# Optimization experiments

Measured on AMD Instinct MI355X. Metric: run time of the kernel, lower is better.

## Reference

```python
import jax, jax.numpy as jnp
import numpy as np

NEG_SLOPE = 0.2

def gat_layer(x, src, dst, W, b, a_src, a_dst, heads, out_dim, concat):
    N = x.shape[0]
    h = (x @ W).reshape(N, heads, out_dim)            # [N,H,D]
    s_src = jnp.sum(h * a_src, axis=-1)               # [N,H]
    s_dst = jnp.sum(h * a_dst, axis=-1)               # [N,H]
    e = jax.nn.leaky_relu(s_src[src] + s_dst[dst], NEG_SLOPE)  # [E,H]
    # segment softmax over destination nodes (self-loops guarantee nonempty segments)
    m = jax.ops.segment_max(e, dst, num_segments=N)
    e = jnp.exp(e - m[dst])
    denom = jax.ops.segment_sum(e, dst, num_segments=N)
    alpha = e / denom[dst]                            # [E,H]
    msg = h[src] * alpha[:, :, None]                  # [E,H,D]
    out = jax.ops.segment_sum(msg, dst, num_segments=N)  # [N,H,D]
    if concat:
        out = out.reshape(N, heads * out_dim)
    else:
        out = out.mean(axis=1)
    return out + b

def setup_inputs() -> dict:
    key = jax.random.key(0)
    ks = jax.random.split(key, 16)
    N, E = 50000, 1600000
    IN, HID, OUT, H = 128, 256, 32, 4
    D = HID // H
    def glorot(k, shape):
        fan = shape[0] + shape[-1]
        return jax.random.uniform(k, shape, jnp.float32, -1.0, 1.0) * np.sqrt(6.0 / fan)
    x = jax.random.normal(ks[0], (N, IN), jnp.float32)
    edge_index = jax.random.randint(ks[1], (2, E), 0, N, jnp.int32)
    return {
        "x": x, "edge_index": edge_index,
        "W0": glorot(ks[2], (IN, H * D)), "b0": jnp.zeros((H * D,), jnp.float32),
        "asrc0": glorot(ks[3], (H, D)), "adst0": glorot(ks[4], (H, D)),
        "W1": glorot(ks[5], (HID, H * D)), "b1": jnp.zeros((H * D,), jnp.float32),
        "asrc1": glorot(ks[6], (H, D)), "adst1": glorot(ks[7], (H, D)),
        "W2": glorot(ks[8], (HID, 1 * OUT)), "b2": jnp.zeros((OUT,), jnp.float32),
        "asrc2": glorot(ks[9], (1, OUT)), "adst2": glorot(ks[10], (1, OUT)),
    }

def reference(x, edge_index, W0, b0, asrc0, adst0, W1, b1, asrc1, adst1, W2, b2, asrc2, adst2):
    N = x.shape[0]
    # add self-loops (PyG GATConv default)
    loop = jnp.arange(N, dtype=edge_index.dtype)
    src = jnp.concatenate([edge_index[0], loop])
    dst = jnp.concatenate([edge_index[1], loop])
    h = gat_layer(x, src, dst, W0, b0, asrc0, adst0, heads=4, out_dim=64, concat=True)
    h = jax.nn.elu(h)
    h = gat_layer(h, src, dst, W1, b1, asrc1, adst1, heads=4, out_dim=64, concat=True)
    h = jax.nn.elu(h)
    h = gat_layer(h, src, dst, W2, b2, asrc2, adst2, heads=1, out_dim=32, concat=False)
    return jax.nn.log_softmax(h, axis=1)
```

## Files before the change

### kernel.cpp

```cpp
#include <hip/hip_runtime.h>
#include <hip/hip_bf16.h>
#include <math.h>

#define IN_DIM 128
#define HID    256
#define OUTD   32
#define HEADS  4
#define NB_SH  7
#define BUCKET_CAP 6144
#define NCHUNK_BLKS 256

typedef __attribute__((ext_vector_type(8))) short s8v;
typedef __attribute__((ext_vector_type(4))) float f4v;

__device__ inline unsigned short f2bf(float f) {
    union { __hip_bfloat16 b; unsigned short u; } cv;
    cv.b = __float2bfloat16(f);
    return cv.u;
}


__global__ __launch_bounds__(256) void csr_hist(const int* __restrict__ ei,
                                                int* __restrict__ H,
                                                int E, int N, int NB, int per_blk) {
    __shared__ int hist[512];
    int t = threadIdx.x;
    for (int i = t; i < NB; i += 256) hist[i] = 0;
    __syncthreads();
    int lo = blockIdx.x * per_blk;
    int hi = min(lo + per_blk, E + N);
    for (int e = lo + t; e < hi; e += 256) {
        int dst = (e < E) ? ei[E + e] : (e - E);
        atomicAdd(&hist[dst >> NB_SH], 1);
    }
    __syncthreads();
    for (int i = t; i < NB; i += 256) H[blockIdx.x * NB + i] = hist[i];
}

__global__ __launch_bounds__(256) void csr_colscan(int* __restrict__ H,
                                                   int* __restrict__ total, int NB) {
    int b = blockIdx.x, t = threadIdx.x;
    int v = H[t * NB + b];
    __shared__ int s[256];
    s[t] = v;
    __syncthreads();
    for (int o = 1; o < 256; o <<= 1) {
        int x = (t >= o) ? s[t - o] : 0;
        __syncthreads();
        s[t] += x;
        __syncthreads();
    }
    H[t * NB + b] = s[t] - v;
    if (t == 255) total[b] = s[255];
}

__global__ void csr_basescan(const int* __restrict__ total, int* __restrict__ base, int NB) {
    __shared__ int s[512];
    int t = threadIdx.x;
    int v = (t < NB) ? total[t] : 0;
    s[t] = v;
    __syncthreads();
    for (int o = 1; o < 512; o <<= 1) {
        int x = (t >= o) ? s[t - o] : 0;
        __syncthreads();
        s[t] += x;
        __syncthreads();
    }
    if (t < NB) base[t] = s[t] - v;
    if (t == NB - 1) base[NB] = s[t];
}

__global__ __launch_bounds__(256) void csr_partition(const int* __restrict__ ei,
                                                     const int* __restrict__ H,
                                                     const int* __restrict__ base,
                                                     int* __restrict__ ebuf,
                                                     int E, int N, int per_blk, int NB) {
    __shared__ int cur[512];
    int t = threadIdx.x;
    for (int i = t; i < NB; i += 256) cur[i] = base[i] + H[blockIdx.x * NB + i];
    __syncthreads();
    int lo = blockIdx.x * per_blk;
    int hi = min(lo + per_blk, E + N);
    for (int e = lo + t; e < hi; e += 256) {
        int src = (e < E) ? ei[e] : (e - E);
        int dst = (e < E) ? ei[E + e] : (e - E);
        int pos = atomicAdd(&cur[dst >> NB_SH], 1);
        ebuf[pos] = src | ((dst & 127) << 16);
    }
}

__global__ __launch_bounds__(256) void csr_sort(const int* __restrict__ ebuf,
                                                const int* __restrict__ base,
                                                int* __restrict__ col,
                                                int* __restrict__ rp, int N, int NB) {
    int b = blockIdx.x, t = threadIdx.x;
    int lo = base[b], hi = base[b + 1];
    int nbase = b << NB_SH;
    __shared__ int c_[128], sc[128], cur[128];
    __shared__ int loc[BUCKET_CAP];
    if (t < 128) c_[t] = 0;
    __syncthreads();
    for (int k = lo + t; k < hi; k += 256) atomicAdd(&c_[(ebuf[k] >> 16) & 127], 1);
    __syncthreads();
    if (t < 128) sc[t] = c_[t];
    __syncthreads();
    for (int o = 1; o < 128; o <<= 1) {
        int x = 0;
        if (t < 128 && t >= o) x = sc[t - o];
        __syncthreads();
        if (t < 128) sc[t] += x;
        __syncthreads();
    }
    if (t < 128) {
        int excl = sc[t] - c_[t];
        cur[t] = excl;
        int node = nbase + t;
        if (node < N) rp[node] = lo + excl;
    }
    if (b == NB - 1 && t == 0) rp[N] = hi;
    __syncthreads();
    for (int k = lo + t; k < hi; k += 256) {
        int e = ebuf[k];
        int p = atomicAdd(&cur[(e >> 16) & 127], 1);
        if (p < BUCKET_CAP) loc[p] = e & 0xFFFF;
    }
    __syncthreads();
    int m = min(hi - lo, BUCKET_CAP);
    for (int k = t; k < m; k += 256) col[lo + k] = loc[k];
}


__global__ __launch_bounds__(256) void prep_w(const float* __restrict__ W,
                                              unsigned short* __restrict__ Wt_h,
                                              unsigned short* __restrict__ Wt_l,
                                              int K, int N) {
    int idx = blockIdx.x * 256 + threadIdx.x;
    if (idx >= K * N) return;
    int n = idx / K, k = idx % K;
    float x = W[(size_t)k * N + n];
    unsigned short h = f2bf(x);
    float hf = __uint_as_float((unsigned)h << 16);
    Wt_h[idx] = h;
    Wt_l[idx] = f2bf(x - hf);
}

__global__ __launch_bounds__(256) void prep_x(const float* __restrict__ X,
                                              unsigned short* __restrict__ Xh,
                                              unsigned short* __restrict__ Xl,
                                              int total8) {
    int idx = blockIdx.x * 256 + threadIdx.x;
    if (idx >= total8) return;
    size_t b = (size_t)idx * 8;
    float4 v0 = *(const float4*)(X + b);
    float4 v1 = *(const float4*)(X + b + 4);
    float x[8] = {v0.x, v0.y, v0.z, v0.w, v1.x, v1.y, v1.z, v1.w};
    union { unsigned short s[8]; uint4 q; } h, l;
#pragma unroll
    for (int j = 0; j < 8; j++) {
        h.s[j] = f2bf(x[j]);
        l.s[j] = f2bf(x[j] - __uint_as_float((unsigned)h.s[j] << 16));
    }
    *(uint4*)(Xh + b) = h.q;
    *(uint4*)(Xl + b) = l.q;
}


template <int BN>
__global__ __launch_bounds__(256, 2) void gemm_mfma(const unsigned short* __restrict__ Ah,
                                                    const unsigned short* __restrict__ Al,
                                                    const unsigned short* __restrict__ Wt_h,
                                                    const unsigned short* __restrict__ Wt_l,
                                                    unsigned short* __restrict__ Cb,
                                                    const float* __restrict__ asrc,
                                                    const float* __restrict__ adst,
                                                    float* __restrict__ ssrcO,
                                                    float* __restrict__ sdstO,
                                                    int M, int K, int Nst, int Hn) {
    constexpr int WROWS = (BN == 128) ? 64 : 32;
    constexpr int WCOLS = (BN == 128) ? 64 : 32;
    constexpr int MI = WROWS / 16, NJ = WCOLS / 16;
    __shared__ unsigned short As_h[128][64], As_l[128][64];
    __shared__ unsigned short Bs_h[BN][64], Bs_l[BN][64];
    int tid = threadIdx.x;
    int lane = tid & 63, w = tid >> 6;
    int wm, wn;
    if (BN == 128) { wm = w & 1; wn = w >> 1; } else { wm = w; wn = 0; }
    int row0 = blockIdx.x * 128, col0 = blockIdx.y * BN;

    f4v acc[MI][NJ];
#pragma unroll
    for (int i = 0; i < MI; i++)
#pragma unroll
        for (int j = 0; j < NJ; j++) acc[i][j] = (f4v)(0.f);

    for (int k0 = 0; k0 < K; k0 += 64) {
#pragma unroll
        for (int i = 0; i < 4; i++) {
            int cidx = tid + i * 256;
            int r = cidx >> 3, ch = cidx & 7;
            int grow = row0 + r;
            uint4 vh = make_uint4(0, 0, 0, 0), vl = make_uint4(0, 0, 0, 0);
            if (grow < M) {
                size_t g = (size_t)grow * K + k0 + ch * 8;
                vh = *(const uint4*)(Ah + g);
                vl = *(const uint4*)(Al + g);
            }
            int chs = ch ^ (r & 7);
            *(uint4*)&As_h[r][chs * 8] = vh;
            *(uint4*)&As_l[r][chs * 8] = vl;
        }
#pragma unroll
        for (int i = 0; i < BN * 8 / 256; i++) {
            int cidx = tid + i * 256;
            int n = cidx >> 3, ch = cidx & 7;
            int chs = ch ^ (n & 7);
            size_t g = (size_t)(col0 + n) * K + k0 + ch * 8;
            *(uint4*)&Bs_h[n][chs * 8] = *(const uint4*)(Wt_h + g);
            *(uint4*)&Bs_l[n][chs * 8] = *(const uint4*)(Wt_l + g);
        }
        __syncthreads();
#pragma unroll
        for (int ks = 0; ks < 2; ks++) {
            s8v ah[MI], al[MI], bh[NJ], bl[NJ];
            int kc = ks * 4 + (lane >> 4);
            int lr = lane & 15;
#pragma unroll
            for (int i = 0; i < MI; i++) {
                int r = wm * WROWS + i * 16 + lr;
                ah[i] = *(const s8v*)&As_h[r][(kc ^ (r & 7)) * 8];
                al[i] = *(const s8v*)&As_l[r][(kc ^ (r & 7)) * 8];
            }
#pragma unroll
            for (int j = 0; j < NJ; j++) {
                int n = wn * WCOLS + j * 16 + lr;
                bh[j] = *(const s8v*)&Bs_h[n][(kc ^ (n & 7)) * 8];
                bl[j] = *(const s8v*)&Bs_l[n][(kc ^ (n & 7)) * 8];
            }
#pragma unroll
            for (int i = 0; i < MI; i++)
#pragma unroll
                for (int j = 0; j < NJ; j++) {
                    acc[i][j] = __builtin_amdgcn_mfma_f32_16x16x32_bf16(ah[i], bh[j], acc[i][j], 0, 0, 0);
                    acc[i][j] = __builtin_amdgcn_mfma_f32_16x16x32_bf16(ah[i], bl[j], acc[i][j], 0, 0, 0);
                    acc[i][j] = __builtin_amdgcn_mfma_f32_16x16x32_bf16(al[i], bh[j], acc[i][j], 0, 0, 0);
                }
        }
        __syncthreads();
    }
    int lr = lane & 15, lg = lane >> 4;
#pragma unroll
    for (int i = 0; i < MI; i++)
#pragma unroll
        for (int j = 0; j < NJ; j++) {
            int gcol = col0 + wn * WCOLS + j * 16 + lr;
#pragma unroll
            for (int rr = 0; rr < 4; rr++) {
                int grow = row0 + wm * WROWS + i * 16 + lg * 4 + rr;
                if (grow < M) Cb[(size_t)grow * Nst + gcol] = f2bf(acc[i][j][rr]);
            }
        }
    int hd = (BN == 128) ? (blockIdx.y * 2 + wn) : 0;
    float as_[NJ], ad_[NJ];
#pragma unroll
    for (int j = 0; j < NJ; j++) {
        int gcol = col0 + wn * WCOLS + j * 16 + lr;
        as_[j] = asrc[gcol];
        ad_[j] = adst[gcol];
    }
#pragma unroll
    for (int i = 0; i < MI; i++)
#pragma unroll
        for (int rr = 0; rr < 4; rr++) {
            float ps = 0.f, pd = 0.f;
#pragma unroll
            for (int j = 0; j < NJ; j++) {
                ps += acc[i][j][rr] * as_[j];
                pd += acc[i][j][rr] * ad_[j];
            }
#pragma unroll
            for (int off = 1; off < 16; off <<= 1) {
                ps += __shfl_xor(ps, off);
                pd += __shfl_xor(pd, off);
            }
            int grow = row0 + wm * WROWS + i * 16 + lg * 4 + rr;
            if (lr == 0 && grow < M) {
                ssrcO[(size_t)grow * Hn + hd] = ps;
                sdstO[(size_t)grow * Hn + hd] = pd;
            }
        }
}


template <int CH, int H, int MODE, int UNR>
__global__ __launch_bounds__(256) void gat_fused(const unsigned short* __restrict__ hb,
                                                 const float* __restrict__ ssrc,
                                                 const float* __restrict__ sdst,
                                                 const int* __restrict__ rp,
                                                 const int* __restrict__ col,
                                                 const float* __restrict__ bias,
                                                 float* __restrict__ outF,
                                                 unsigned short* __restrict__ outH,
                                                 unsigned short* __restrict__ outL, int N) {
    const int TPE = CH / 8;
    const int EPW = 64 / TPE;
    const int D = CH / H;
    constexpr int SHCH = (CH == 256) ? 9 : 6;
    constexpr int SHS = (H == 4) ? 4 : 2;
    int wv = threadIdx.x >> 6, lane = threadIdx.x & 63;
    int n = blockIdx.x * 4 + wv;
    if (n >= N) return;
    int k0 = __builtin_amdgcn_readfirstlane(rp[n]);
    int k1 = __builtin_amdgcn_readfirstlane(rp[n + 1]);

    int h1 = lane % H;
    int slot = lane / H;
    const int SL = 64 / H;
    float sd1 = sdst[(size_t)n * H + h1];
    float m = -1e30f, l = 0.f;
    for (int k = k0 + slot; k < k1; k += SL) {
        int s = col[k];
        float e = ssrc[(size_t)s * H + h1] + sd1;
        e = (e > 0.f) ? e : 0.2f * e;
        float mn = fmaxf(m, e);
        l = l * __expf(m - mn) + __expf(e - mn);
        m = mn;
    }
#pragma unroll
    for (int off = H; off < 64; off <<= 1) {
        float m2 = __shfl_xor(m, off);
        float l2 = __shfl_xor(l, off);
        float mn = fmaxf(m, m2);
        l = l * __expf(m - mn) + l2 * __expf(m2 - mn);
        m = mn;
    }

    int eo = lane / TPE;
    int c = (lane % TPE) * 8;
    int head = c / D;
    float mh = __shfl(m, head);
    float invl = 1.f / __shfl(l, head);
    float sdh = __shfl(sd1, head);

    const char* hbc = (const char*)hb;
    const char* ssc = (const char*)ssrc;
    unsigned cb = (unsigned)(c << 1);
    unsigned hb4 = (unsigned)(head << 2);

    float acc[8];
#pragma unroll
    for (int j = 0; j < 8; j++) acc[j] = 0.f;

    for (int k = k0; k < k1; k += UNR * EPW) {
        int ss[UNR];
        float aa[UNR];
#pragma unroll
        for (int u = 0; u < UNR; u++) {
            int ku = k + u * EPW + eo;
            bool v = ku < k1;
            ss[u] = col[v ? ku : k0];
            aa[u] = v ? invl : 0.f;
        }
        uint4 hv[UNR];
#pragma unroll
        for (int u = 0; u < UNR; u++)
            hv[u] = *(const uint4*)(hbc + (((unsigned)ss[u] << SHCH) + cb));
#pragma unroll
        for (int u = 0; u < UNR; u++) {
            float e = *(const float*)(ssc + (((unsigned)ss[u] << SHS) + hb4)) + sdh;
            e = (e > 0.f) ? e : 0.2f * e;
            aa[u] *= __expf(e - mh);
        }
#pragma unroll
        for (int u = 0; u < UNR; u++) {
            const unsigned* p = (const unsigned*)&hv[u];
#pragma unroll
            for (int q = 0; q < 4; q++) {
                acc[2 * q]     += aa[u] * __uint_as_float(p[q] << 16);
                acc[2 * q + 1] += aa[u] * __uint_as_float(p[q] & 0xffff0000u);
            }
        }
    }
#pragma unroll
    for (int off = TPE; off < 64; off <<= 1)
#pragma unroll
        for (int j = 0; j < 8; j++) acc[j] += __shfl_xor(acc[j], off);

    float o[8];
#pragma unroll
    for (int j = 0; j < 8; j++) o[j] = acc[j] + bias[c + j];
    if (MODE == 1) {
        float mx = o[0];
#pragma unroll
        for (int j = 1; j < 8; j++) mx = fmaxf(mx, o[j]);
#pragma unroll
        for (int off = 1; off < TPE; off <<= 1) mx = fmaxf(mx, __shfl_xor(mx, off));
        float sm = 0.f;
#pragma unroll
        for (int j = 0; j < 8; j++) sm += __expf(o[j] - mx);
#pragma unroll
        for (int off = 1; off < TPE; off <<= 1) sm += __shfl_xor(sm, off);
        float lg = logf(sm) + mx;
        if (eo != 0) return;
        float4* op = (float4*)(outF + (size_t)n * CH + c);
        op[0] = make_float4(o[0] - lg, o[1] - lg, o[2] - lg, o[3] - lg);
        op[1] = make_float4(o[4] - lg, o[5] - lg, o[6] - lg, o[7] - lg);
    } else {
        if (eo != 0) return;
        union { unsigned short s[8]; uint4 q; } ph, pl;
#pragma unroll
        for (int j = 0; j < 8; j++) {
            float v = (o[j] > 0.f) ? o[j] : expm1f(o[j]);
            ph.s[j] = f2bf(v);
            pl.s[j] = f2bf(v - __uint_as_float((unsigned)ph.s[j] << 16));
        }
        *(uint4*)(outH + (size_t)n * CH + c) = ph.q;
        *(uint4*)(outL + (size_t)n * CH + c) = pl.q;
    }
}


extern "C" void kernel_launch(void* const* d_in, const int* in_sizes, int n_in,
                              void* d_out, int out_size, void* d_ws, size_t ws_size,
                              hipStream_t stream) {
    const float* x   = (const float*)d_in[0];
    const int*   ei  = (const int*)d_in[1];
    const float* W0  = (const float*)d_in[2];
    const float* b0  = (const float*)d_in[3];
    const float* as0 = (const float*)d_in[4];
    const float* ad0 = (const float*)d_in[5];
    const float* W1  = (const float*)d_in[6];
    const float* b1  = (const float*)d_in[7];
    const float* as1 = (const float*)d_in[8];
    const float* ad1 = (const float*)d_in[9];
    const float* W2  = (const float*)d_in[10];
    const float* b2  = (const float*)d_in[11];
    const float* as2 = (const float*)d_in[12];
    const float* ad2 = (const float*)d_in[13];

    int N = in_sizes[0] / IN_DIM;
    int E = in_sizes[1] / 2;
    int Et = E + N;
    int NB = (N + 127) >> NB_SH;

    char* w = (char*)d_ws;
    size_t off = 0;
    auto alloc = [&](size_t bytes) -> void* {
        void* p = w + off;
        off = (off + bytes + 255) & ~(size_t)255;
        return p;
    };
    unsigned short* Qh    = (unsigned short*)alloc((size_t)N * HID * 2);
    unsigned short* Ql    = (unsigned short*)alloc((size_t)N * HID * 2);
    unsigned short* Ab    = (unsigned short*)alloc((size_t)N * HID * 2);
    unsigned short* xh    = (unsigned short*)alloc((size_t)N * IN_DIM * 2);
    unsigned short* xl    = (unsigned short*)alloc((size_t)N * IN_DIM * 2);
    float*          ssrc  = (float*)alloc((size_t)N * HEADS * 4);
    float*          sdst  = (float*)alloc((size_t)N * HEADS * 4);
    int*            rp    = (int*)alloc((size_t)(N + 1) * 4);
    int*            col   = (int*)alloc((size_t)Et * 4);
    int*            H     = (int*)alloc((size_t)NCHUNK_BLKS * NB * 4);
    int*            total = (int*)alloc((size_t)(NB + 1) * 4);
    int*            base  = (int*)alloc((size_t)(NB + 1) * 4);
    int*            ebuf  = (int*)alloc((size_t)Et * 4);
    unsigned short* Wt0h  = (unsigned short*)alloc((size_t)IN_DIM * HID * 2);
    unsigned short* Wt0l  = (unsigned short*)alloc((size_t)IN_DIM * HID * 2);
    unsigned short* Wt1h  = (unsigned short*)alloc((size_t)HID * HID * 2);
    unsigned short* Wt1l  = (unsigned short*)alloc((size_t)HID * HID * 2);
    unsigned short* Wt2h  = (unsigned short*)alloc((size_t)HID * OUTD * 2);
    unsigned short* Wt2l  = (unsigned short*)alloc((size_t)HID * OUTD * 2);

    prep_w<<<(IN_DIM * HID + 255) / 256, 256, 0, stream>>>(W0, Wt0h, Wt0l, IN_DIM, HID);
    prep_w<<<(HID * HID + 255) / 256, 256, 0, stream>>>(W1, Wt1h, Wt1l, HID, HID);
    prep_w<<<(HID * OUTD + 255) / 256, 256, 0, stream>>>(W2, Wt2h, Wt2l, HID, OUTD);
    int t8 = N * IN_DIM / 8;
    prep_x<<<(t8 + 255) / 256, 256, 0, stream>>>(x, xh, xl, t8);

    int per_blk = (Et + NCHUNK_BLKS - 1) / NCHUNK_BLKS;
    csr_hist<<<NCHUNK_BLKS, 256, 0, stream>>>(ei, H, E, N, NB, per_blk);
    csr_colscan<<<NB, 256, 0, stream>>>(H, total, NB);
    csr_basescan<<<1, 512, 0, stream>>>(total, base, NB);
    csr_partition<<<NCHUNK_BLKS, 256, 0, stream>>>(ei, H, base, ebuf, E, N, per_blk, NB);
    csr_sort<<<NB, 256, 0, stream>>>(ebuf, base, col, rp, N, NB);

    dim3 gm((N + 127) / 128, 2);
    dim3 gm2((N + 127) / 128, 1);
    int gg = (N + 3) / 4;

    gemm_mfma<128><<<gm, 256, 0, stream>>>(xh, xl, Wt0h, Wt0l, Ab, as0, ad0, ssrc, sdst,
                                           N, IN_DIM, HID, HEADS);
    gat_fused<HID, HEADS, 0, 6><<<gg, 256, 0, stream>>>(Ab, ssrc, sdst, rp, col, b0,
                                                        nullptr, Qh, Ql, N);

    gemm_mfma<128><<<gm, 256, 0, stream>>>(Qh, Ql, Wt1h, Wt1l, Ab, as1, ad1, ssrc, sdst,
                                           N, HID, HID, HEADS);
    gat_fused<HID, HEADS, 0, 6><<<gg, 256, 0, stream>>>(Ab, ssrc, sdst, rp, col, b1,
                                                        nullptr, Qh, Ql, N);

    gemm_mfma<32><<<gm2, 256, 0, stream>>>(Qh, Ql, Wt2h, Wt2l, Ab, as2, ad2, ssrc, sdst,
                                           N, HID, OUTD, 1);
    gat_fused<OUTD, 1, 1, 2><<<gg, 256, 0, stream>>>(Ab, ssrc, sdst, rp, col, b2,
                                                     (float*)d_out, nullptr, nullptr, N);
}
```

Baseline: 430.3 us.

## Process attention heads sequentially per wave in fused GAT aggregation

The aggregation kernel now loops over heads, and within each head the wave's lanes cover only that head's D features, so more edges are processed per pass (TPE = D/8 instead of CH/8). Each lane loads one head's score per edge rather than mixing heads across lanes, and the unroll factor for the hidden layers drops from 6 to 2. The edge list and column indices are now re-read once per head, adding more load instructions and more loop overhead. In exchange, each pass covers more edges in parallel, and smaller rows may improve locality per head.

```diff
diff --git a/kernel.cpp b/kernel.cpp
--- a/kernel.cpp
+++ b/kernel.cpp
@@ -301,11 +301,9 @@
                                                  float* __restrict__ outF,
                                                  unsigned short* __restrict__ outH,
                                                  unsigned short* __restrict__ outL, int N) {
-    const int TPE = CH / 8;
+    const int D = CH / H;
+    const int TPE = D / 8;
     const int EPW = 64 / TPE;
-    const int D = CH / H;
-    constexpr int SHCH = (CH == 256) ? 9 : 6;
-    constexpr int SHS = (H == 4) ? 4 : 2;
     int wv = threadIdx.x >> 6, lane = threadIdx.x & 63;
     int n = blockIdx.x * 4 + wv;
     if (n >= N) return;
@@ -335,86 +333,87 @@
     }
 
     int eo = lane / TPE;
-    int c = (lane % TPE) * 8;
-    int head = c / D;
-    float mh = __shfl(m, head);
-    float invl = 1.f / __shfl(l, head);
-    float sdh = __shfl(sd1, head);
-
-    const char* hbc = (const char*)hb;
-    const char* ssc = (const char*)ssrc;
-    unsigned cb = (unsigned)(c << 1);
-    unsigned hb4 = (unsigned)(head << 2);
-
-    float acc[8];
-#pragma unroll
-    for (int j = 0; j < 8; j++) acc[j] = 0.f;
-
-    for (int k = k0; k < k1; k += UNR * EPW) {
-        int ss[UNR];
-        float aa[UNR];
-#pragma unroll
-        for (int u = 0; u < UNR; u++) {
-            int ku = k + u * EPW + eo;
-            bool v = ku < k1;
-            ss[u] = col[v ? ku : k0];
-            aa[u] = v ? invl : 0.f;
-        }
-        uint4 hv[UNR];
-#pragma unroll
-        for (int u = 0; u < UNR; u++)
-            hv[u] = *(const uint4*)(hbc + (((unsigned)ss[u] << SHCH) + cb));
-#pragma unroll
-        for (int u = 0; u < UNR; u++) {
-            float e = *(const float*)(ssc + (((unsigned)ss[u] << SHS) + hb4)) + sdh;
-            e = (e > 0.f) ? e : 0.2f * e;
-            aa[u] *= __expf(e - mh);
-        }
-#pragma unroll
-        for (int u = 0; u < UNR; u++) {
-            const unsigned* p = (const unsigned*)&hv[u];
-#pragma unroll
-            for (int q = 0; q < 4; q++) {
-                acc[2 * q]     += aa[u] * __uint_as_float(p[q] << 16);
-                acc[2 * q + 1] += aa[u] * __uint_as_float(p[q] & 0xffff0000u);
-            }
-        }
-    }
-#pragma unroll
-    for (int off = TPE; off < 64; off <<= 1)
-#pragma unroll
-        for (int j = 0; j < 8; j++) acc[j] += __shfl_xor(acc[j], off);
-
-    float o[8];
-#pragma unroll
-    for (int j = 0; j < 8; j++) o[j] = acc[j] + bias[c + j];
-    if (MODE == 1) {
-        float mx = o[0];
-#pragma unroll
-        for (int j = 1; j < 8; j++) mx = fmaxf(mx, o[j]);
-#pragma unroll
-        for (int off = 1; off < TPE; off <<= 1) mx = fmaxf(mx, __shfl_xor(mx, off));
-        float sm = 0.f;
-#pragma unroll
-        for (int j = 0; j < 8; j++) sm += __expf(o[j] - mx);
-#pragma unroll
-        for (int off = 1; off < TPE; off <<= 1) sm += __shfl_xor(sm, off);
-        float lg = logf(sm) + mx;
-        if (eo != 0) return;
-        float4* op = (float4*)(outF + (size_t)n * CH + c);
-        op[0] = make_float4(o[0] - lg, o[1] - lg, o[2] - lg, o[3] - lg);
-        op[1] = make_float4(o[4] - lg, o[5] - lg, o[6] - lg, o[7] - lg);
-    } else {
-        if (eo != 0) return;
-        union { unsigned short s[8]; uint4 q; } ph, pl;
-#pragma unroll
-        for (int j = 0; j < 8; j++) {
-            float v = (o[j] > 0.f) ? o[j] : expm1f(o[j]);
-            ph.s[j] = f2bf(v);
-            pl.s[j] = f2bf(v - __uint_as_float((unsigned)ph.s[j] << 16));
-        }
-        *(uint4*)(outH + (size_t)n * CH + c) = ph.q;
-        *(uint4*)(outL + (size_t)n * CH + c) = pl.q;
+    int cl = (lane % TPE) * 8;
+
+    for (int hd = 0; hd < H; hd++) {
+        float mh = __shfl(m, hd);
+        float invl = 1.f / __shfl(l, hd);
+        float sdh = __shfl(sd1, hd);
+        int c = hd * D + cl;
+
+        float acc[8];
+#pragma unroll
+        for (int j = 0; j < 8; j++) acc[j] = 0.f;
+
+        for (int k = k0; k < k1; k += UNR * EPW) {
+            int ss[UNR];
+            float aa[UNR];
+#pragma unroll
+            for (int u = 0; u < UNR; u++) {
+                int ku = k + u * EPW + eo;
+                bool v = ku < k1;
+                ss[u] = col[v ? ku : k0];
+                aa[u] = v ? invl : 0.f;
+            }
+            uint4 hv[UNR];
+#pragma unroll
+            for (int u = 0; u < UNR; u++)
+                hv[u] = *(const uint4*)(hb + (size_t)ss[u] * CH + c);
+#pragma unroll
+            for (int u = 0; u < UNR; u++) {
+                float e = ssrc[(size_t)ss[u] * H + hd] + sdh;
+                e = (e > 0.f) ? e : 0.2f * e;
+                aa[u] *= __expf(e - mh);
+            }
+#pragma unroll
+            for (int u = 0; u < UNR; u++) {
+                const unsigned* p = (const unsigned*)&hv[u];
+#pragma unroll
+                for (int q = 0; q < 4; q++) {
+                    acc[2 * q]     += aa[u] * __uint_as_float(p[q] << 16);
+                    acc[2 * q + 1] += aa[u] * __uint_as_float(p[q] & 0xffff0000u);
+                }
+            }
+        }
+#pragma unroll
+        for (int off = TPE; off < 64; off <<= 1)
+#pragma unroll
+            for (int j = 0; j < 8; j++) acc[j] += __shfl_xor(acc[j], off);
+
+        if (MODE == 1) {
+            float o[8];
+#pragma unroll
+            for (int j = 0; j < 8; j++) o[j] = acc[j] + bias[c + j];
+            float mx = o[0];
+#pragma unroll
+            for (int j = 1; j < 8; j++) mx = fmaxf(mx, o[j]);
+#pragma unroll
+            for (int off = 1; off < TPE; off <<= 1) mx = fmaxf(mx, __shfl_xor(mx, off));
+            float sm = 0.f;
+#pragma unroll
+            for (int j = 0; j < 8; j++) sm += __expf(o[j] - mx);
+#pragma unroll
+            for (int off = 1; off < TPE; off <<= 1) sm += __shfl_xor(sm, off);
+            float lg = logf(sm) + mx;
+            if (eo == 0) {
+                float4* op = (float4*)(outF + (size_t)n * CH + c);
+                op[0] = make_float4(o[0] - lg, o[1] - lg, o[2] - lg, o[3] - lg);
+                op[1] = make_float4(o[4] - lg, o[5] - lg, o[6] - lg, o[7] - lg);
+            }
+        } else {
+            if (eo == 0) {
+                union { unsigned short s[8]; uint4 q; } ph, pl;
+#pragma unroll
+                for (int j = 0; j < 8; j++) {
+                    float v = acc[j] + bias[c + j];
+                    v = (v > 0.f) ? v : expm1f(v);
+                    ph.s[j] = f2bf(v);
+                    pl.s[j] = f2bf(v - __uint_as_float((unsigned)ph.s[j] << 16));
+                }
+                *(uint4*)(outH + (size_t)n * CH + c) = ph.q;
+                *(uint4*)(outL + (size_t)n * CH + c) = pl.q;
+            }
+        }
     }
 }
 
@@ -488,12 +487,12 @@
 
     gemm_mfma<128><<<gm, 256, 0, stream>>>(xh, xl, Wt0h, Wt0l, Ab, as0, ad0, ssrc, sdst,
                                            N, IN_DIM, HID, HEADS);
-    gat_fused<HID, HEADS, 0, 6><<<gg, 256, 0, stream>>>(Ab, ssrc, sdst, rp, col, b0,
+    gat_fused<HID, HEADS, 0, 2><<<gg, 256, 0, stream>>>(Ab, ssrc, sdst, rp, col, b0,
                                                         nullptr, Qh, Ql, N);
 
     gemm_mfma<128><<<gm, 256, 0, stream>>>(Qh, Ql, Wt1h, Wt1l, Ab, as1, ad1, ssrc, sdst,
                                            N, HID, HID, HEADS);
-    gat_fused<HID, HEADS, 0, 6><<<gg, 256, 0, stream>>>(Ab, ssrc, sdst, rp, col, b1,
+    gat_fused<HID, HEADS, 0, 2><<<gg, 256, 0, stream>>>(Ab, ssrc, sdst, rp, col, b1,
                                                         nullptr, Qh, Ql, N);
 
     gemm_mfma<32><<<gm2, 256, 0, stream>>>(Qh, Ql, Wt2h, Wt2l, Ab, as2, ad2, ssrc, sdst,
```

After: 547.6 us. 27.3% more time.

## Sort CSR column indices by source range within each destination row

Applied to the files above, without the earlier changes.

The bucket sort in csr_sort now keys on (destination node, coarse source bin), so neighbor lists inside each row are grouped by source-index range. The aim is better cache locality for the gathers of source features in the aggregation kernels. The counting array grows to 128*64 shared ints, and the scan becomes a 256-thread block scan over 32-entry chunks, which adds some sort cost. The gat_fused template parameter for the two hidden layers also drops from 6 to 4.

```diff
diff --git a/kernel.cpp b/kernel.cpp
--- a/kernel.cpp
+++ b/kernel.cpp
@@ -9,6 +9,8 @@
 #define NB_SH  7
 #define BUCKET_CAP 6144
 #define NCHUNK_BLKS 256
+#define SRC_SH 10
+#define KSRC   64
 
 typedef __attribute__((ext_vector_type(8))) short s8v;
 typedef __attribute__((ext_vector_type(4))) float f4v;
@@ -96,32 +98,47 @@
     int b = blockIdx.x, t = threadIdx.x;
     int lo = base[b], hi = base[b + 1];
     int nbase = b << NB_SH;
-    __shared__ int c_[128], sc[128], cur[128];
+    __shared__ int cnt[128 * KSRC];
     __shared__ int loc[BUCKET_CAP];
-    if (t < 128) c_[t] = 0;
-    __syncthreads();
-    for (int k = lo + t; k < hi; k += 256) atomicAdd(&c_[(ebuf[k] >> 16) & 127], 1);
-    __syncthreads();
-    if (t < 128) sc[t] = c_[t];
-    __syncthreads();
-    for (int o = 1; o < 128; o <<= 1) {
-        int x = 0;
-        if (t < 128 && t >= o) x = sc[t - o];
-        __syncthreads();
-        if (t < 128) sc[t] += x;
-        __syncthreads();
-    }
-    if (t < 128) {
-        int excl = sc[t] - c_[t];
-        cur[t] = excl;
-        int node = nbase + t;
-        if (node < N) rp[node] = lo + excl;
-    }
-    if (b == NB - 1 && t == 0) rp[N] = hi;
+    __shared__ int ssum[256];
+    for (int i = t; i < 128 * KSRC; i += 256) cnt[i] = 0;
     __syncthreads();
     for (int k = lo + t; k < hi; k += 256) {
         int e = ebuf[k];
-        int p = atomicAdd(&cur[(e >> 16) & 127], 1);
+        int key = ((e >> 16) & 127) * KSRC + ((e & 0xFFFF) >> SRC_SH);
+        atomicAdd(&cnt[key], 1);
+    }
+    __syncthreads();
+    int base_i = t * 32;
+    int s = 0;
+#pragma unroll
+    for (int i = 0; i < 32; i++) s += cnt[base_i + i];
+    ssum[t] = s;
+    __syncthreads();
+    for (int o = 1; o < 256; o <<= 1) {
+        int x = (t >= o) ? ssum[t - o] : 0;
+        __syncthreads();
+        ssum[t] += x;
+        __syncthreads();
+    }
+    int run = (t == 0) ? 0 : ssum[t - 1];
+#pragma unroll
+    for (int i = 0; i < 32; i++) {
+        int c = cnt[base_i + i];
+        cnt[base_i + i] = run;
+        run += c;
+    }
+    __syncthreads();
+    if (t < 128) {
+        int node = nbase + t;
+        if (node < N) rp[node] = lo + cnt[t * KSRC];
+    }
+    if (b == NB - 1 && t == 0) rp[N] = hi;
+    __syncthreads();
+    for (int k = lo + t; k < hi; k += 256) {
+        int e = ebuf[k];
+        int key = ((e >> 16) & 127) * KSRC + ((e & 0xFFFF) >> SRC_SH);
+        int p = atomicAdd(&cnt[key], 1);
         if (p < BUCKET_CAP) loc[p] = e & 0xFFFF;
     }
     __syncthreads();
@@ -488,12 +505,12 @@
 
     gemm_mfma<128><<<gm, 256, 0, stream>>>(xh, xl, Wt0h, Wt0l, Ab, as0, ad0, ssrc, sdst,
                                            N, IN_DIM, HID, HEADS);
-    gat_fused<HID, HEADS, 0, 6><<<gg, 256, 0, stream>>>(Ab, ssrc, sdst, rp, col, b0,
+    gat_fused<HID, HEADS, 0, 4><<<gg, 256, 0, stream>>>(Ab, ssrc, sdst, rp, col, b0,
                                                         nullptr, Qh, Ql, N);
 
     gemm_mfma<128><<<gm, 256, 0, stream>>>(Qh, Ql, Wt1h, Wt1l, Ab, as1, ad1, ssrc, sdst,
                                            N, HID, HID, HEADS);
-    gat_fused<HID, HEADS, 0, 6><<<gg, 256, 0, stream>>>(Ab, ssrc, sdst, rp, col, b1,
+    gat_fused<HID, HEADS, 0, 4><<<gg, 256, 0, stream>>>(Ab, ssrc, sdst, rp, col, b1,
                                                         nullptr, Qh, Ql, N);
 
     gemm_mfma<32><<<gm2, 256, 0, stream>>>(Qh, Ql, Wt2h, Wt2l, Ab, as2, ad2, ssrc, sdst,
```

After: 429.0 us. Within noise of the previous version (-0.3%).
